# Optimization experiments

Hardware: AMD Instinct MI355X
Metric: run time of the kernel (lower is better)

## Reference

```python
import jax, jax.numpy as jnp
import numpy as np

N_PATHS = 65536
N_STEPS = 512
DT = 1.0 / 252.0
KAPPA = 2.72
THETA = -3.5
SIGMA_P = (0.1 + 1.6) / 2.0  # stop_gradient((diff_min+diff_max)/2)
RHO = -0.85
R = 0.0373
LAMBDA_MAX = 3.0
LOG_V_MIN = -7.0
LOG_V_MAX = 2.0


def setup_inputs() -> dict:
    key = jax.random.key(0)
    ks = jax.random.split(key, 8)
    # eqx.nn.Linear default init: U(-1/sqrt(fan_in), 1/sqrt(fan_in))
    def lin(k, shape):
        fan_in = shape[-1]
        lim = 1.0 / np.sqrt(fan_in)
        return jax.random.uniform(k, shape, jnp.float32, -lim, lim)
    return {
        "z1": jax.random.normal(ks[0], (N_PATHS, N_STEPS), jnp.float32),
        "z2": jax.random.normal(ks[1], (N_PATHS, N_STEPS), jnp.float32),
        "W1": lin(ks[2], (32, 2)),
        "b1": lin(ks[3], (32,)),
        "W2": lin(ks[4], (32, 32)),
        "b2": lin(ks[5], (32,)),
        "W3": lin(ks[6], (1, 32)),
        "b3": lin(ks[7], (1,)),
        "init_log_v": jnp.float32(THETA),
    }


def _girsanov_lambda(log_v, t_scalar, W1, b1, W2, b2, W3, b3):
    # Batched MLP(2->32->32->1) with gelu, tanh-bounded output. log_v: (P,)
    x = jnp.stack([log_v, jnp.full_like(log_v, t_scalar)], axis=-1)  # (P, 2)
    h = jax.nn.gelu(x @ W1.T + b1)
    h = jax.nn.gelu(h @ W2.T + b2)
    raw = (h @ W3.T + b3)[:, 0]  # (P,)
    return LAMBDA_MAX * jnp.tanh(raw)


def reference(z1, z2, W1, b1, W2, b2, W3, b3, init_log_v):
    sqrt_dt = jnp.sqrt(jnp.float32(DT))
    dW_v = sqrt_dt * z1                                     # (P, S)
    dW_s = RHO * dW_v + jnp.sqrt(1.0 - RHO ** 2) * sqrt_dt * z2
    t_idx = jnp.arange(N_STEPS, dtype=jnp.float32) * DT / (N_STEPS * DT)

    # Batched scan over time; carry holds all paths at once (vmap-equivalent).
    def scan_fn(carry, inputs):
        log_v, log_s, lam_sq = carry                        # each (P,)
        dw_v_t, dw_s_t, t_n = inputs
        mu_p = KAPPA * (THETA - log_v) * DT
        lam = _girsanov_lambda(log_v, t_n, W1, b1, W2, b2, W3, b3)
        drift_q = mu_p - lam * SIGMA_P * DT
        log_v_next = jnp.clip(log_v + drift_q + SIGMA_P * dw_v_t, LOG_V_MIN, LOG_V_MAX)
        ev = jnp.exp(log_v)
        vol = jnp.sqrt(jnp.maximum(ev, 1e-10))
        log_s_next = log_s + (R - 0.5 * ev) * DT + vol * dw_s_t
        lam_sq = lam_sq + lam ** 2 * DT
        return (log_v_next, log_s_next, lam_sq), (log_v_next, log_s_next)

    p = z1.shape[0]
    init = (jnp.full((p,), init_log_v, jnp.float32),
            jnp.zeros((p,), jnp.float32),
            jnp.zeros((p,), jnp.float32))
    xs = (dW_v.T, dW_s.T, t_idx)                            # time-major
    (_, _, lambda_sq), (lv_path, ls_path) = jax.lax.scan(scan_fn, init, xs)
    log_v_paths = lv_path.T                                 # (P, S)
    spot_paths = jnp.exp(ls_path.T)                         # (P, S), normalized by S0
    return log_v_paths, spot_paths, lambda_sq
```

## Files before the change

kernel.cpp:

```cpp
#include <hip/hip_runtime.h>
#include <math.h>

#define NPATHS 65536
#define NSTEPS 512

__device__ __forceinline__ float gelu_fast(float x) {
    float x2 = x * x;
    float u = 1.5957691216057308f * x * fmaf(0.044715f, x2, 1.0f);
    float e = __expf(-u);
    return x * __builtin_amdgcn_rcpf(1.0f + e);
}

extern "C" __global__ void __launch_bounds__(256, 1)
sde_kernel(const float* __restrict__ z1, const float* __restrict__ z2,
           const float* __restrict__ W1, const float* __restrict__ b1,
           const float* __restrict__ W2, const float* __restrict__ b2,
           const float* __restrict__ W3, const float* __restrict__ b3,
           const float* __restrict__ init_log_v,
           float* __restrict__ out)
{
    __shared__ float sW1[64];
    __shared__ float sb1[32];
    __shared__ float sW2[1024];
    __shared__ float sb2[32];
    __shared__ float sW3[32];
    __shared__ float sb3[1];

    const int tid = threadIdx.x;
    for (int i = tid; i < 1024; i += 256) sW2[i] = W2[i];
    if (tid < 64) sW1[tid] = W1[tid];
    if (tid < 32) { sb1[tid] = b1[tid]; sb2[tid] = b2[tid]; sW3[tid] = W3[tid]; }
    if (tid == 0) sb3[0] = b3[0];
    __syncthreads();

    const int p = blockIdx.x * 256 + tid;

    const float DTf = 1.0f / 252.0f;
    const float sqrt_dt = sqrtf(DTf);
    const float c_dws2 = sqrtf(0.2775f) * sqrt_dt;

    float log_v = init_log_v[0];
    float log_s = 0.0f;
    float lam_sq = 0.0f;

    const float* z1p = z1 + (size_t)p * NSTEPS;
    const float* z2p = z2 + (size_t)p * NSTEPS;
    float* out_lv = out + (size_t)p * NSTEPS;
    float* out_sp = out + (size_t)NPATHS * NSTEPS + (size_t)p * NSTEPS;
    float* out_lamsq = out + (size_t)NPATHS * NSTEPS * 2;

    for (int n = 0; n < NSTEPS; ++n) {
        float z1e = z1p[n];
        float z2e = z2p[n];

        float tn = ((float)n * DTf) / 2.0317460317460316f;

        float dwv = sqrt_dt * z1e;
        float dws = (-0.85f) * dwv + c_dws2 * z2e;

        float h1[32];
        #pragma unroll
        for (int j = 0; j < 32; ++j) {
            float pre = fmaf(sW1[2*j], log_v, fmaf(sW1[2*j+1], tn, sb1[j]));
            h1[j] = gelu_fast(pre);
        }
        float raw = sb3[0];
        #pragma unroll
        for (int j = 0; j < 32; ++j) {
            float acc = sb2[j];
            #pragma unroll
            for (int i = 0; i < 32; ++i)
                acc = fmaf(h1[i], sW2[32*j + i], acc);
            raw = fmaf(gelu_fast(acc), sW3[j], raw);
        }
        float e2 = __expf(2.0f * raw);
        float lam = 3.0f * (1.0f - 2.0f * __builtin_amdgcn_rcpf(1.0f + e2));

        float mu_p = (2.72f * (-3.5f - log_v)) * DTf;
        float drift_q = mu_p - (lam * 0.85f) * DTf;
        float lvn = log_v + drift_q + 0.85f * dwv;
        lvn = fminf(fmaxf(lvn, -7.0f), 2.0f);

        float ev = expf(log_v);
        float vol = sqrtf(fmaxf(ev, 1e-10f));
        float lsn = log_s + (0.0373f - 0.5f * ev) * DTf + vol * dws;

        lam_sq = lam_sq + (lam * lam) * DTf;

        log_v = lvn;
        log_s = lsn;

        out_lv[n] = lvn;
        out_sp[n] = expf(lsn);
    }
    out_lamsq[p] = lam_sq;
}

extern "C" void kernel_launch(void* const* d_in, const int* in_sizes, int n_in,
                              void* d_out, int out_size, void* d_ws, size_t ws_size,
                              hipStream_t stream) {
    const float* z1  = (const float*)d_in[0];
    const float* z2  = (const float*)d_in[1];
    const float* W1  = (const float*)d_in[2];
    const float* b1  = (const float*)d_in[3];
    const float* W2  = (const float*)d_in[4];
    const float* b2  = (const float*)d_in[5];
    const float* W3  = (const float*)d_in[6];
    const float* b3  = (const float*)d_in[7];
    const float* ilv = (const float*)d_in[8];

    dim3 grid(NPATHS / 256);
    dim3 block(256);
    hipLaunchKernelGGL(sde_kernel, grid, block, 0, stream,
                       z1, z2, W1, b1, W2, b2, W3, b3, ilv, (float*)d_out);
}
```

Baseline: 5.313 ms.

## Vectorize per-path loads/stores to float4 and use float4 LDS weight reads

Each thread now processes four time steps per iteration, loading z1/z2 as float4 and writing both output paths as float4. Weight reads from shared memory use float4 (W2) and float2 (W1) vector loads, and the outer hidden-layer loop is only partially unrolled. This targets per-element global memory transactions and LDS instruction count, but reshapes register use and code size in the compute-bound MLP.

```diff
diff --git a/kernel.cpp b/kernel.cpp
--- a/kernel.cpp
+++ b/kernel.cpp
@@ -3,6 +3,7 @@
 
 #define NPATHS 65536
 #define NSTEPS 512
+#define T 4
 
 __device__ __forceinline__ float gelu_fast(float x) {
     float x2 = x * x;
@@ -19,18 +20,18 @@
            const float* __restrict__ init_log_v,
            float* __restrict__ out)
 {
-    __shared__ float sW1[64];
-    __shared__ float sb1[32];
-    __shared__ float sW2[1024];
-    __shared__ float sb2[32];
-    __shared__ float sW3[32];
-    __shared__ float sb3[1];
+    __shared__ float4 sW2v[256];
+    __shared__ float2 sW1v[32];
+    __shared__ float  sb1[32], sb2[32], sW3[32];
+    __shared__ float  sb3;
 
     const int tid = threadIdx.x;
-    for (int i = tid; i < 1024; i += 256) sW2[i] = W2[i];
-    if (tid < 64) sW1[tid] = W1[tid];
-    if (tid < 32) { sb1[tid] = b1[tid]; sb2[tid] = b2[tid]; sW3[tid] = W3[tid]; }
-    if (tid == 0) sb3[0] = b3[0];
+    sW2v[tid] = ((const float4*)W2)[tid];
+    if (tid < 32) {
+        sW1v[tid] = ((const float2*)W1)[tid];
+        sb1[tid] = b1[tid]; sb2[tid] = b2[tid]; sW3[tid] = W3[tid];
+    }
+    if (tid == 0) sb3 = b3[0];
     __syncthreads();
 
     const int p = blockIdx.x * 256 + tid;
@@ -43,16 +44,13 @@
     float log_s = 0.0f;
     float lam_sq = 0.0f;
 
-    const float* z1p = z1 + (size_t)p * NSTEPS;
-    const float* z2p = z2 + (size_t)p * NSTEPS;
-    float* out_lv = out + (size_t)p * NSTEPS;
-    float* out_sp = out + (size_t)NPATHS * NSTEPS + (size_t)p * NSTEPS;
+    const float4* z1p = (const float4*)(z1 + (size_t)p * NSTEPS);
+    const float4* z2p = (const float4*)(z2 + (size_t)p * NSTEPS);
+    float4* out_lv = (float4*)(out + (size_t)p * NSTEPS);
+    float4* out_sp = (float4*)(out + (size_t)NPATHS * NSTEPS + (size_t)p * NSTEPS);
     float* out_lamsq = out + (size_t)NPATHS * NSTEPS * 2;
 
-    for (int n = 0; n < NSTEPS; ++n) {
-        float z1e = z1p[n];
-        float z2e = z2p[n];
-
+    auto step = [&](int n, float z1e, float z2e, float& lvout, float& spout) {
         float tn = ((float)n * DTf) / 2.0317460317460316f;
 
         float dwv = sqrt_dt * z1e;
@@ -61,16 +59,21 @@
         float h1[32];
         #pragma unroll
         for (int j = 0; j < 32; ++j) {
-            float pre = fmaf(sW1[2*j], log_v, fmaf(sW1[2*j+1], tn, sb1[j]));
-            h1[j] = gelu_fast(pre);
+            float2 w = sW1v[j];
+            h1[j] = gelu_fast(fmaf(w.x, log_v, fmaf(w.y, tn, sb1[j])));
         }
-        float raw = sb3[0];
-        #pragma unroll
+        float raw = sb3;
+        #pragma unroll 4
         for (int j = 0; j < 32; ++j) {
             float acc = sb2[j];
             #pragma unroll
-            for (int i = 0; i < 32; ++i)
-                acc = fmaf(h1[i], sW2[32*j + i], acc);
+            for (int q = 0; q < 8; ++q) {
+                float4 w = sW2v[j * 8 + q];
+                acc = fmaf(h1[4*q + 0], w.x, acc);
+                acc = fmaf(h1[4*q + 1], w.y, acc);
+                acc = fmaf(h1[4*q + 2], w.z, acc);
+                acc = fmaf(h1[4*q + 3], w.w, acc);
+            }
             raw = fmaf(gelu_fast(acc), sW3[j], raw);
         }
         float e2 = __expf(2.0f * raw);
@@ -90,8 +93,22 @@
         log_v = lvn;
         log_s = lsn;
 
-        out_lv[n] = lvn;
-        out_sp[n] = expf(lsn);
+        lvout = lvn;
+        spout = expf(lsn);
+    };
+
+    for (int n0 = 0; n0 < NSTEPS; n0 += T) {
+        float4 za = z1p[n0 / 4];
+        float4 zb = z2p[n0 / 4];
+
+        float4 lvb, spb;
+        step(n0 + 0, za.x, zb.x, lvb.x, spb.x);
+        step(n0 + 1, za.y, zb.y, lvb.y, spb.y);
+        step(n0 + 2, za.z, zb.z, lvb.z, spb.z);
+        step(n0 + 3, za.w, zb.w, lvb.w, spb.w);
+
+        out_lv[n0 / 4] = lvb;
+        out_sp[n0 / 4] = spb;
     }
     out_lamsq[p] = lam_sq;
 }
```

New measurement: 5.293 ms. About the same (-0.4%).
